# Performance work log

Measured on AMD Instinct MI355X. Metric: run time of the kernel, lower is better.

## Reference

```python
import jax, jax.numpy as jnp
import numpy as np

NEG_SLOPE = 0.2  # LeakyReLU slope

N, E, D_IN, D_OUT, H, NBIN = 50000, 500000, 256, 256, 8, 10
DH = D_OUT // H


def setup_inputs() -> dict:
    key = jax.random.key(0)
    ks = jax.random.split(key, 9)
    emb_rel = jax.random.normal(ks[0], (N, D_IN), dtype=jnp.float32)
    head_idxs = jax.random.randint(ks[1], (E,), 0, N, dtype=jnp.int32)
    tail_idxs = jax.random.randint(ks[2], (E,), 0, N, dtype=jnp.int32)
    bins = jax.random.randint(ks[3], (E,), 0, NBIN, dtype=jnp.int32)
    # xavier-normal-ish scaled params (gain for relu)
    attn_proj_w = jax.random.normal(ks[4], (D_OUT, 2 * D_IN), dtype=jnp.float32) * (1.4142 * (2.0 / (2 * D_IN + D_OUT)) ** 0.5)
    attn_proj_b = jnp.zeros((D_OUT,), dtype=jnp.float32)
    attn_bin = jax.random.normal(ks[5], (NBIN, H, 1), dtype=jnp.float32) * 0.3
    attn_vec = jax.random.normal(ks[6], (1, H, DH), dtype=jnp.float32) * (1.4142 * (2.0 / (H + DH)) ** 0.5)
    aggr_proj_w = jax.random.normal(ks[7], (D_OUT, D_IN), dtype=jnp.float32) * (1.4142 * (2.0 / (D_IN + D_OUT)) ** 0.5)
    aggr_proj_b = jnp.zeros((D_OUT,), dtype=jnp.float32)
    return {
        "emb_rel": emb_rel,
        "head_idxs": head_idxs,
        "tail_idxs": tail_idxs,
        "bins": bins,
        "attn_proj_w": attn_proj_w,
        "attn_proj_b": attn_proj_b,
        "attn_bin": attn_bin,
        "attn_vec": attn_vec,
        "aggr_proj_w": aggr_proj_w,
        "aggr_proj_b": aggr_proj_b,
        "num_nodes": N,
    }


def reference(emb_rel, head_idxs, tail_idxs, bins, attn_proj_w, attn_proj_b,
              attn_bin, attn_vec, aggr_proj_w, aggr_proj_b, num_nodes):
    num_head, dim_hid = attn_vec.shape[1], attn_vec.shape[2]
    eh = emb_rel[head_idxs]                      # (E, D_in)
    et = emb_rel[tail_idxs]                      # (E, D_in)
    concat = jnp.concatenate([eh, et], axis=-1)  # (E, 2*D_in)
    proj = (concat @ attn_proj_w.T + attn_proj_b).reshape(-1, num_head, dim_hid)
    lrelu = jnp.where(proj >= 0, proj, NEG_SLOPE * proj)
    # raw attention logits per edge/head: (E, H, 1)
    attn_raw = jnp.sum(lrelu * attn_vec, axis=-1, keepdims=True) + attn_bin[bins]
    # segmented softmax over edges grouped by head node
    seg_max = jax.ops.segment_max(attn_raw, head_idxs, num_segments=num_nodes)
    seg_max = jnp.where(jnp.isfinite(seg_max), seg_max, 0.0)  # empty segments -> 0 (never gathered anyway)
    attn_val = jnp.exp(attn_raw - seg_max[head_idxs])
    attn_sums = jax.ops.segment_sum(attn_val, head_idxs, num_segments=num_nodes)
    beta = attn_val / (attn_sums[head_idxs] + 1e-16)            # (E, H, 1)
    aggr = (et @ aggr_proj_w.T + aggr_proj_b).reshape(-1, num_head, dim_hid)
    out = jax.ops.segment_sum(beta * aggr, head_idxs, num_segments=num_nodes)
    return out.reshape(num_nodes, num_head * dim_hid)
```

## Files before the change

### kernel.cpp

```cpp
#include <hip/hip_runtime.h>
#include <math.h>

#define D_IN 256
#define D_OUT 256
#define NH 8
#define DH 32
#define NBIN 10
#define NEG_SLOPE 0.2f
#define CAP 96

typedef short short8 __attribute__((ext_vector_type(8)));
typedef float f32x4 __attribute__((ext_vector_type(4)));

__device__ __forceinline__ unsigned short f2bf(float f) {
  unsigned u = __float_as_uint(f);
  unsigned r = u + 0x7fffu + ((u >> 16) & 1u);
  return (unsigned short)(r >> 16);
}
__device__ __forceinline__ float bf2f(unsigned short s) {
  return __uint_as_float((unsigned)s << 16);
}

__global__ void prep_kernel(const float* __restrict__ attn_w,
                            const float* __restrict__ attn_b,
                            const float* __restrict__ aggr_w,
                            const float* __restrict__ aggr_b,
                            const float* __restrict__ emb,
                            unsigned short* __restrict__ WCbf,
                            float* __restrict__ biasC,
                            unsigned short* __restrict__ embbf,
                            int* __restrict__ cnt, int N) {
  const int b = blockIdx.x, k = threadIdx.x;
  if (b < 768) {
    const int j = b;
    int idx0 = j * 256 + k;
    if (idx0 < N) cnt[idx0] = 0;
    float v, bia = 0.f;
    if (j < 256) {
      v = attn_w[j * 512 + k];
    } else {
      int idx = j - 256, g = idx >> 3, r = idx & 7;
      if (r < 4) { int c = g * 4 + r;     v = attn_w[c * 512 + 256 + k]; bia = attn_b[c]; }
      else       { int c = g * 4 + r - 4; v = aggr_w[c * 256 + k];       bia = aggr_b[c]; }
    }
    WCbf[j * 256 + k] = f2bf(v);
    if (k == 0) biasC[j] = bia;
  } else {
    const long long total = (long long)N * 256;
    long long i = (((long long)(b - 768)) * 256 + k) * 8;
    if (i >= total) return;
    float4 a = *(const float4*)(emb + i);
    float4 c = *(const float4*)(emb + i + 4);
    short8 o;
    o[0] = (short)f2bf(a.x); o[1] = (short)f2bf(a.y);
    o[2] = (short)f2bf(a.z); o[3] = (short)f2bf(a.w);
    o[4] = (short)f2bf(c.x); o[5] = (short)f2bf(c.y);
    o[6] = (short)f2bf(c.z); o[7] = (short)f2bf(c.w);
    *(short8*)(embbf + i) = o;
  }
}

#define EPAD 36
__global__ __launch_bounds__(256) void gemm_bf16_kernel(
    const unsigned short* __restrict__ Abf,
    const unsigned short* __restrict__ Bbf,
    const float* __restrict__ biasC,
    float* __restrict__ P1, unsigned short* __restrict__ P2A, int N) {
  __shared__ char smem[128 * EPAD * 4];
  unsigned short* As = (unsigned short*)smem;
  unsigned short* Bs = (unsigned short*)(smem + 8192);
  float* Ls = (float*)smem;
  const int tid = threadIdx.x;
  const int row0 = blockIdx.y * 128, col0 = blockIdx.x * 128;
  const int wave = tid >> 6, l = tid & 63;
  const int wm = wave >> 1, wn = wave & 1;
  const int lr = l & 15;
  const int lq = l >> 4;
  const int srow = tid >> 2;
  const int sk = (tid & 3) * 8;
  f32x4 acc[4][4] = {};
  for (int kk = 0; kk < 256; kk += 32) {
    int ar0 = row0 + srow;      if (ar0 >= N) ar0 = N - 1;
    int ar1 = row0 + 64 + srow; if (ar1 >= N) ar1 = N - 1;
    short8 a0 = *(const short8*)(Abf + (size_t)ar0 * 256 + kk + sk);
    short8 a1 = *(const short8*)(Abf + (size_t)ar1 * 256 + kk + sk);
    short8 b0 = *(const short8*)(Bbf + (size_t)(col0 + srow) * 256 + kk + sk);
    short8 b1 = *(const short8*)(Bbf + (size_t)(col0 + 64 + srow) * 256 + kk + sk);
    __syncthreads();
    *(short8*)&As[srow * 32 + sk] = a0;
    *(short8*)&As[(64 + srow) * 32 + sk] = a1;
    *(short8*)&Bs[srow * 32 + sk] = b0;
    *(short8*)&Bs[(64 + srow) * 32 + sk] = b1;
    __syncthreads();
    short8 af[4], bfr[4];
#pragma unroll
    for (int i = 0; i < 4; ++i)
      af[i] = *(const short8*)&As[(wm * 64 + i * 16 + lr) * 32 + lq * 8];
#pragma unroll
    for (int j = 0; j < 4; ++j)
      bfr[j] = *(const short8*)&Bs[(wn * 64 + j * 16 + lr) * 32 + lq * 8];
#pragma unroll
    for (int i = 0; i < 4; ++i)
#pragma unroll
      for (int j = 0; j < 4; ++j)
        acc[i][j] = __builtin_amdgcn_mfma_f32_16x16x32_bf16(af[i], bfr[j], acc[i][j], 0, 0, 0);
  }
  for (int j = 0; j < 4; ++j) {
    __syncthreads();
    const float bias = biasC[col0 + wn * 64 + j * 16 + lr];
#pragma unroll
    for (int i = 0; i < 4; ++i) {
      const int lrow = wm * 64 + i * 16 + lq * 4;
#pragma unroll
      for (int r = 0; r < 4; ++r)
        Ls[(lrow + r) * EPAD + wn * 16 + lr] = acc[i][j][r] + bias;
    }
    __syncthreads();
    if (col0 < 256) {
      const int sub = tid & 7, half = sub >> 2, quad = sub & 3;
#pragma unroll
      for (int s = 0; s < 4; ++s) {
        const int row = (tid >> 3) + s * 32;
        const int grow = row0 + row;
        if (grow < N) {
          float4 v = *(const float4*)&Ls[row * EPAD + half * 16 + quad * 4];
          *(float4*)(P1 + (size_t)grow * 256 + col0 + half * 64 + j * 16 + quad * 4) = v;
        }
      }
    } else {
      const int o = tid & 3, half = o >> 1, part = o & 1;
#pragma unroll
      for (int s = 0; s < 2; ++s) {
        const int row = (tid >> 2) + s * 64;
        const int grow = row0 + row;
        if (grow < N) {
          const float* src = &Ls[row * EPAD + half * 16 + part * 8];
          short8 v;
#pragma unroll
          for (int q = 0; q < 8; ++q) v[q] = (short)f2bf(src[q]);
          *(short8*)(P2A + (size_t)grow * 512 + (col0 - 256) + half * 64 + j * 16 + part * 8) = v;
        }
      }
    }
  }
}

__global__ void bucket_scatter_kernel(const int* __restrict__ head,
                                      const int* __restrict__ tail,
                                      const int* __restrict__ bins,
                                      int* __restrict__ cnt,
                                      int* __restrict__ bucket, int E) {
  int e = blockIdx.x * blockDim.x + threadIdx.x;
  if (e >= E) return;
  int h = head[e];
  int slot = atomicAdd(&cnt[h], 1);
  if (slot < CAP) bucket[(size_t)h * CAP + slot] = (bins[e] << 16) | tail[e];
}

__global__ __launch_bounds__(256) void node_aggr_kernel(
    const float* __restrict__ P1, const unsigned short* __restrict__ P2A,
    const int* __restrict__ cnt, const int* __restrict__ bucket,
    const float* __restrict__ attn_vec, const float* __restrict__ attn_bin,
    float* __restrict__ out, int N) {
  __shared__ float sbin[NBIN * NH];
  const int tid = threadIdx.x;
  if (tid < NBIN * NH) sbin[tid] = attn_bin[tid];
  __syncthreads();
  const int n = blockIdx.x * 4 + (tid >> 6);
  if (n >= N) return;
  const int l = tid & 63;
  const int h = l >> 3;
  const float4 av = *(const float4*)(attn_vec + l * 4);
  const float4 p1 = *(const float4*)(P1 + (size_t)n * 256 + l * 4);
  const int* brow = bucket + (size_t)n * CAP;
  int d = cnt[n];
  if (d > CAP) d = CAP;
  float m = -INFINITY, sum = 0.f;
  float4 acc = make_float4(0.f, 0.f, 0.f, 0.f);
  int pk = 0;
  short8 cur = {};
  if (d > 0) {
    pk = brow[0];
    cur = *(const short8*)(P2A + (size_t)(pk & 0xFFFF) * 512 + l * 8);
  }
  for (int i = 0; i < d; ++i) {
    const int ni = (i + 1 < d) ? i + 1 : i;
    const int pk_next = brow[ni];
    const short8 nxt = *(const short8*)(P2A + (size_t)(pk_next & 0xFFFF) * 512 + l * 8);
    const int bin = pk >> 16;
    float s = 0.f, x;
    x = p1.x + bf2f((unsigned short)cur[0]); x = (x >= 0.f) ? x : NEG_SLOPE * x; s += x * av.x;
    x = p1.y + bf2f((unsigned short)cur[1]); x = (x >= 0.f) ? x : NEG_SLOPE * x; s += x * av.y;
    x = p1.z + bf2f((unsigned short)cur[2]); x = (x >= 0.f) ? x : NEG_SLOPE * x; s += x * av.z;
    x = p1.w + bf2f((unsigned short)cur[3]); x = (x >= 0.f) ? x : NEG_SLOPE * x; s += x * av.w;
    s += __shfl_down(s, 4, 8);
    s += __shfl_down(s, 2, 8);
    s += __shfl_down(s, 1, 8);
    s = __shfl(s, 0, 8);
    const float logit = s + sbin[bin * NH + h];
    const float mn = fmaxf(m, logit);
    const float scale = __expf(m - mn);
    const float w = __expf(logit - mn);
    sum = sum * scale + w;
    acc.x = acc.x * scale + w * bf2f((unsigned short)cur[4]);
    acc.y = acc.y * scale + w * bf2f((unsigned short)cur[5]);
    acc.z = acc.z * scale + w * bf2f((unsigned short)cur[6]);
    acc.w = acc.w * scale + w * bf2f((unsigned short)cur[7]);
    m = mn;
    pk = pk_next;
    cur = nxt;
  }
  const float inv = 1.f / (sum + 1e-16f);
  float4 o;
  o.x = acc.x * inv; o.y = acc.y * inv; o.z = acc.z * inv; o.w = acc.w * inv;
  *(float4*)(out + (size_t)n * 256 + l * 4) = o;
}

extern "C" void kernel_launch(void* const* d_in, const int* in_sizes, int n_in,
                              void* d_out, int out_size, void* d_ws, size_t ws_size,
                              hipStream_t stream) {
  const float* emb      = (const float*)d_in[0];
  const int*   head     = (const int*)d_in[1];
  const int*   tail     = (const int*)d_in[2];
  const int*   bins     = (const int*)d_in[3];
  const float* attn_w   = (const float*)d_in[4];
  const float* attn_b   = (const float*)d_in[5];
  const float* attn_bin = (const float*)d_in[6];
  const float* attn_vec = (const float*)d_in[7];
  const float* aggr_w   = (const float*)d_in[8];
  const float* aggr_b   = (const float*)d_in[9];
  float* out = (float*)d_out;

  const int N = in_sizes[0] / D_IN;
  const int E = in_sizes[1];

  char* ws = (char*)d_ws;
  size_t off = 0;
  auto walloc = [&](size_t bytes) -> void* {
    void* p = ws + off;
    off += (bytes + 255) & ~(size_t)255;
    return p;
  };
  float*          P1     = (float*)walloc((size_t)N * 256 * sizeof(float));
  unsigned short* P2A    = (unsigned short*)walloc((size_t)N * 512 * sizeof(short));
  unsigned short* embbf  = (unsigned short*)walloc((size_t)N * 256 * sizeof(short));
  unsigned short* WCbf   = (unsigned short*)walloc((size_t)768 * 256 * sizeof(short));
  float*          biasC  = (float*)walloc(768 * sizeof(float));
  int*            cnt    = (int*)walloc((size_t)N * sizeof(int));
  int*            bucket = (int*)walloc((size_t)N * CAP * sizeof(int));

  const int conv_blocks = (int)(((long long)N * 256 / 8 + 255) / 256);
  prep_kernel<<<768 + conv_blocks, 256, 0, stream>>>(attn_w, attn_b, aggr_w, aggr_b,
                                                     emb, WCbf, biasC, embbf, cnt, N);

  dim3 ggrid(768 / 128, (N + 127) / 128);
  gemm_bf16_kernel<<<ggrid, 256, 0, stream>>>(embbf, WCbf, biasC, P1, P2A, N);

  bucket_scatter_kernel<<<(E + 255) / 256, 256, 0, stream>>>(head, tail, bins, cnt, bucket, E);

  node_aggr_kernel<<<(N + 3) / 4, 256, 0, stream>>>(P1, P2A, cnt, bucket,
                                                    attn_vec, attn_bin, out, N);
}
```

Baseline: 290.1 us.

## Rework node aggregation softmax with lazy rescaling, exp2, swizzle reductions and two-edge unroll

Rewrites the per-node online softmax loop so it handles two edges per iteration with a deeper prefetch of gathered rows. It folds log2(e) into the attention vector and bin table so it can use native exp2, and it rescales the accumulator only when a logit exceeds the running max by a threshold. Head-lane reductions use ds_swizzle instead of shuffles, and the node index is made wave-uniform. This cuts exp and rescale work plus reduction latency and exposes more memory-level parallelism. The cost is more registers and an accumulator that can grow by up to 2^8 before renormalising.

```diff
diff --git a/kernel.cpp b/kernel.cpp
--- a/kernel.cpp
+++ b/kernel.cpp
@@ -8,6 +8,8 @@
 #define NBIN 10
 #define NEG_SLOPE 0.2f
 #define CAP 96
+#define LOG2E 1.4426950408889634f
+#define THR 8.0f
 
 typedef short short8 __attribute__((ext_vector_type(8)));
 typedef float f32x4 __attribute__((ext_vector_type(4)));
@@ -157,6 +159,36 @@
   if (slot < CAP) bucket[(size_t)h * CAP + slot] = (bins[e] << 16) | tail[e];
 }
 
+template <int PAT>
+__device__ __forceinline__ float swz_add(float s) {
+  return s + __uint_as_float(
+      (unsigned)__builtin_amdgcn_ds_swizzle((int)__float_as_uint(s), PAT));
+}
+
+__device__ __forceinline__ short8 ldP2A(const unsigned short* __restrict__ P2A,
+                                        int t, int l8) {
+  return *(const short8*)(P2A + ((size_t)(t & 0xFFFF) << 9) + l8);
+}
+
+__device__ __forceinline__ float edge_dot(short8 c, float4 p1, float4 av) {
+  float x, s;
+  x = p1.x + bf2f((unsigned short)c[0]); s  = fmaxf(x, NEG_SLOPE * x) * av.x;
+  x = p1.y + bf2f((unsigned short)c[1]); s += fmaxf(x, NEG_SLOPE * x) * av.y;
+  x = p1.z + bf2f((unsigned short)c[2]); s += fmaxf(x, NEG_SLOPE * x) * av.z;
+  x = p1.w + bf2f((unsigned short)c[3]); s += fmaxf(x, NEG_SLOPE * x) * av.w;
+  s = swz_add<0x041F>(s);
+  s = swz_add<0x081F>(s);
+  s = swz_add<0x101F>(s);
+  return s;
+}
+
+__device__ __forceinline__ float4 edge_val(short8 c) {
+  float4 v;
+  v.x = bf2f((unsigned short)c[4]); v.y = bf2f((unsigned short)c[5]);
+  v.z = bf2f((unsigned short)c[6]); v.w = bf2f((unsigned short)c[7]);
+  return v;
+}
+
 __global__ __launch_bounds__(256) void node_aggr_kernel(
     const float* __restrict__ P1, const unsigned short* __restrict__ P2A,
     const int* __restrict__ cnt, const int* __restrict__ bucket,
@@ -164,56 +196,80 @@
     float* __restrict__ out, int N) {
   __shared__ float sbin[NBIN * NH];
   const int tid = threadIdx.x;
-  if (tid < NBIN * NH) sbin[tid] = attn_bin[tid];
+  if (tid < NBIN * NH) sbin[tid] = attn_bin[tid] * LOG2E;
   __syncthreads();
-  const int n = blockIdx.x * 4 + (tid >> 6);
-  if (n >= N) return;
+  const int nu = __builtin_amdgcn_readfirstlane(blockIdx.x * 4 + (tid >> 6));
+  if (nu >= N) return;
   const int l = tid & 63;
+  const int l8 = l * 8;
   const int h = l >> 3;
-  const float4 av = *(const float4*)(attn_vec + l * 4);
-  const float4 p1 = *(const float4*)(P1 + (size_t)n * 256 + l * 4);
-  const int* brow = bucket + (size_t)n * CAP;
-  int d = cnt[n];
+  float4 av = *(const float4*)(attn_vec + l * 4);
+  av.x *= LOG2E; av.y *= LOG2E; av.z *= LOG2E; av.w *= LOG2E;
+  const float4 p1 = *(const float4*)(P1 + (size_t)nu * 256 + l * 4);
+  const int* brow = bucket + (size_t)nu * CAP;
+  int d = cnt[nu];
   if (d > CAP) d = CAP;
-  float m = -INFINITY, sum = 0.f;
+  float m = 0.f, m8 = 0.f, sum = 0.f;
   float4 acc = make_float4(0.f, 0.f, 0.f, 0.f);
-  int pk = 0;
-  short8 cur = {};
   if (d > 0) {
-    pk = brow[0];
-    cur = *(const short8*)(P2A + (size_t)(pk & 0xFFFF) * 512 + l * 8);
-  }
-  for (int i = 0; i < d; ++i) {
-    const int ni = (i + 1 < d) ? i + 1 : i;
-    const int pk_next = brow[ni];
-    const short8 nxt = *(const short8*)(P2A + (size_t)(pk_next & 0xFFFF) * 512 + l * 8);
-    const int bin = pk >> 16;
-    float s = 0.f, x;
-    x = p1.x + bf2f((unsigned short)cur[0]); x = (x >= 0.f) ? x : NEG_SLOPE * x; s += x * av.x;
-    x = p1.y + bf2f((unsigned short)cur[1]); x = (x >= 0.f) ? x : NEG_SLOPE * x; s += x * av.y;
-    x = p1.z + bf2f((unsigned short)cur[2]); x = (x >= 0.f) ? x : NEG_SLOPE * x; s += x * av.z;
-    x = p1.w + bf2f((unsigned short)cur[3]); x = (x >= 0.f) ? x : NEG_SLOPE * x; s += x * av.w;
-    s += __shfl_down(s, 4, 8);
-    s += __shfl_down(s, 2, 8);
-    s += __shfl_down(s, 1, 8);
-    s = __shfl(s, 0, 8);
-    const float logit = s + sbin[bin * NH + h];
-    const float mn = fmaxf(m, logit);
-    const float scale = __expf(m - mn);
-    const float w = __expf(logit - mn);
-    sum = sum * scale + w;
-    acc.x = acc.x * scale + w * bf2f((unsigned short)cur[4]);
-    acc.y = acc.y * scale + w * bf2f((unsigned short)cur[5]);
-    acc.z = acc.z * scale + w * bf2f((unsigned short)cur[6]);
-    acc.w = acc.w * scale + w * bf2f((unsigned short)cur[7]);
-    m = mn;
-    pk = pk_next;
-    cur = nxt;
+    const int dm1 = d - 1;
+    const int t0 = brow[0];
+    short8 c0 = ldP2A(P2A, t0, l8);
+    int tA = brow[1 <= dm1 ? 1 : dm1];
+    int tB = brow[2 <= dm1 ? 2 : dm1];
+    short8 cA = ldP2A(P2A, tA, l8);
+    short8 cB = ldP2A(P2A, tB, l8);
+    m = edge_dot(c0, p1, av) + sbin[(t0 >> 16) * NH + h];
+    m8 = m + THR;
+    sum = 1.f;
+    float4 v0 = edge_val(c0);
+    acc.x = v0.x; acc.y = v0.y; acc.z = v0.z; acc.w = v0.w;
+    int i = 1;
+    for (; i + 1 < d; i += 2) {
+      const int jC = (i + 2 <= dm1) ? i + 2 : dm1;
+      const int jD = (i + 3 <= dm1) ? i + 3 : dm1;
+      const int tC = brow[jC];
+      const int tD = brow[jD];
+      short8 cC = ldP2A(P2A, tC, l8);
+      short8 cD = ldP2A(P2A, tD, l8);
+      const float lA = edge_dot(cA, p1, av) + sbin[(tA >> 16) * NH + h];
+      const float lB = edge_dot(cB, p1, av) + sbin[(tB >> 16) * NH + h];
+      const float lmax = fmaxf(lA, lB);
+      if (__any(lmax > m8)) {
+        const float mn = fmaxf(m, lmax);
+        const float sc = __builtin_amdgcn_exp2f(m - mn);
+        sum *= sc; acc.x *= sc; acc.y *= sc; acc.z *= sc; acc.w *= sc;
+        m = mn; m8 = mn + THR;
+      }
+      const float wA = __builtin_amdgcn_exp2f(lA - m);
+      const float wB = __builtin_amdgcn_exp2f(lB - m);
+      sum += wA + wB;
+      const float4 vA = edge_val(cA), vB = edge_val(cB);
+      acc.x += wA * vA.x + wB * vB.x;
+      acc.y += wA * vA.y + wB * vB.y;
+      acc.z += wA * vA.z + wB * vB.z;
+      acc.w += wA * vA.w + wB * vB.w;
+      tA = tC; cA = cC; tB = tD; cB = cD;
+    }
+    if (i < d) {
+      const float lA = edge_dot(cA, p1, av) + sbin[(tA >> 16) * NH + h];
+      if (__any(lA > m8)) {
+        const float mn = fmaxf(m, lA);
+        const float sc = __builtin_amdgcn_exp2f(m - mn);
+        sum *= sc; acc.x *= sc; acc.y *= sc; acc.z *= sc; acc.w *= sc;
+        m = mn;
+      }
+      const float wA = __builtin_amdgcn_exp2f(lA - m);
+      sum += wA;
+      const float4 vA = edge_val(cA);
+      acc.x += wA * vA.x; acc.y += wA * vA.y;
+      acc.z += wA * vA.z; acc.w += wA * vA.w;
+    }
   }
   const float inv = 1.f / (sum + 1e-16f);
   float4 o;
   o.x = acc.x * inv; o.y = acc.y * inv; o.z = acc.z * inv; o.w = acc.w * inv;
-  *(float4*)(out + (size_t)n * 256 + l * 4) = o;
+  *(float4*)(out + (size_t)nu * 256 + l * 4) = o;
 }
 
 extern "C" void kernel_launch(void* const* d_in, const int* in_sizes, int n_in,
```

Result: no change. 290.4 us (+0.1%).
